# Optimization experiments

Hardware: AMD Instinct MI355X
Metric: run time of the kernel (lower is better)

## Reference

```python
import jax, jax.numpy as jnp
import numpy as np
from jax.ops import segment_sum

NUM_NODES = 100000
NUM_GRAPHS = 256


def gcn_conv(x, src, dst, W, b, num_nodes):
    """PyG GCNConv: add self-loops, symmetric deg^-1/2 normalization,
    out = scatter_add(norm * (xW)[src]) + b."""
    h = x @ W  # [N, H]
    loop = jnp.arange(num_nodes, dtype=src.dtype)
    s = jnp.concatenate([src, loop])
    d = jnp.concatenate([dst, loop])
    deg = segment_sum(jnp.ones_like(d, dtype=h.dtype), d, num_segments=num_nodes)
    dinv = jnp.where(deg > 0, jax.lax.rsqrt(deg), 0.0)
    norm = dinv[s] * dinv[d]  # [E+N]
    msg = h[s] * norm[:, None]
    return segment_sum(msg, d, num_segments=num_nodes) + b


def global_mean_pool(x, batch, num_graphs):
    summed = segment_sum(x, batch, num_segments=num_graphs)
    cnt = segment_sum(jnp.ones_like(batch, dtype=x.dtype), batch, num_segments=num_graphs)
    return summed / jnp.maximum(cnt, 1.0)[:, None]


def setup_inputs() -> dict:
    key = jax.random.key(0)
    ks = jax.random.split(key, 8)
    N, E, F_in, H = NUM_NODES, 3200000, 128, 64
    x = jax.random.normal(ks[0], (N, F_in), dtype=jnp.float32)
    edge_index = jax.random.randint(ks[1], (2, E), 0, N, dtype=jnp.int64)
    batch = jnp.sort(jax.random.randint(ks[2], (N,), 0, NUM_GRAPHS, dtype=jnp.int64))
    def glorot(k, shape):
        fan = shape[0] + shape[1]
        return jax.random.uniform(k, shape, jnp.float32, -1.0, 1.0) * np.sqrt(6.0 / fan)
    return {
        "x": x, "edge_index": edge_index, "batch": batch,
        "W1": glorot(ks[3], (F_in, H)), "b1": jnp.zeros((H,), jnp.float32),
        "W2": glorot(ks[4], (H, H)),   "b2": jnp.zeros((H,), jnp.float32),
        "W3": glorot(ks[5], (H, H)),   "b3": jnp.zeros((H,), jnp.float32),
        "Wl": glorot(ks[6], (H, 2)),   "bl": jnp.zeros((2,), jnp.float32),
    }


def reference(x, edge_index, batch, W1, b1, W2, b2, W3, b3, Wl, bl):
    src, dst = edge_index[0], edge_index[1]
    # Dropout acts as identity in eval mode; reference is deterministic.
    h = jax.nn.relu(gcn_conv(x, src, dst, W1, b1, NUM_NODES))
    h = jax.nn.relu(gcn_conv(h, src, dst, W2, b2, NUM_NODES))
    h = jax.nn.relu(gcn_conv(h, src, dst, W3, b3, NUM_NODES))
    g = global_mean_pool(h, batch, NUM_GRAPHS)  # [G, H]
    return g @ Wl + bl  # [G, 2]
```

## Files before the change

kernel.cpp:

```cpp
#include <hip/hip_runtime.h>
#include <hip/hip_bf16.h>
#include <cstdint>
#include <cstddef>

static constexpr int N_NODES = 100000;
static constexpr int N_GRAPHS = 256;
static constexpr int HF = 64;

#define SCAN_T 256
#define SCAN_E 8
#define SCAN_CHUNK (SCAN_T * SCAN_E)

#define BSHIFT 9
#define BNODES 512
#define ECHUNK 4096
#define SRCBITS 17

typedef unsigned short u16;
typedef unsigned int u32;
typedef unsigned long long u64;

__global__ void scan1_k(const int* __restrict__ in, int* __restrict__ out,
                        int* __restrict__ sums, int n) {
    __shared__ int lds[SCAN_T];
    int t = threadIdx.x;
    int base = blockIdx.x * SCAN_CHUNK + t * SCAN_E;
    int v[SCAN_E];
    int s = 0;
#pragma unroll
    for (int i = 0; i < SCAN_E; ++i) {
        int idx = base + i;
        int x = (idx < n) ? in[idx] : 0;
        v[i] = s; s += x;
    }
    lds[t] = s; __syncthreads();
    for (int off = 1; off < SCAN_T; off <<= 1) {
        int a = (t >= off) ? lds[t - off] : 0;
        __syncthreads();
        lds[t] += a;
        __syncthreads();
    }
    int excl = (t == 0) ? 0 : lds[t - 1];
    if (t == SCAN_T - 1) sums[blockIdx.x] = lds[SCAN_T - 1];
#pragma unroll
    for (int i = 0; i < SCAN_E; ++i) {
        int idx = base + i;
        if (idx < n) out[idx] = excl + v[i];
    }
}

__global__ void scan2_k(int* __restrict__ sums, int nb) {
    __shared__ int lds[SCAN_T];
    int t = threadIdx.x;
    lds[t] = (t < nb) ? sums[t] : 0;
    __syncthreads();
    for (int off = 1; off < SCAN_T; off <<= 1) {
        int a = (t >= off) ? lds[t - off] : 0;
        __syncthreads();
        lds[t] += a;
        __syncthreads();
    }
    int excl = (t == 0) ? 0 : lds[t - 1];
    if (t < nb) sums[t] = excl;
}

__global__ void scan3_k(int* __restrict__ out, const int* __restrict__ sums, int n) {
    int idx = blockIdx.x * blockDim.x + threadIdx.x;
    if (idx < n) out[idx] += sums[idx / SCAN_CHUNK];
}

__global__ void bhist_k(const int* __restrict__ dst, int* __restrict__ cnt,
                        int E, int nblk, int NB) {
    __shared__ int c[256];
    int t = threadIdx.x;
    c[t] = 0;
    __syncthreads();
    int base = blockIdx.x * ECHUNK;
    int m = min(ECHUNK, E - base);
    for (int i = t; i < m; i += 256) atomicAdd(&c[dst[base + i] >> BSHIFT], 1);
    __syncthreads();
    if (t < NB) cnt[t * nblk + blockIdx.x] = c[t];
}

__global__ void scatter_k(const int* __restrict__ src, const int* __restrict__ dst,
                          const int* __restrict__ scn, int* __restrict__ es,
                          int E, int nblk, int NB) {
    __shared__ int offs[256];
    int t = threadIdx.x;
    if (t < NB) offs[t] = scn[t * nblk + blockIdx.x];
    __syncthreads();
    int base = blockIdx.x * ECHUNK;
    int m = min(ECHUNK, E - base);
    for (int i = t; i < m; i += 256) {
        int e = base + i;
        int d = dst[e];
        int b = d >> BSHIFT;
        int p = atomicAdd(&offs[b], 1);
        es[p] = ((d & (BNODES - 1)) << SRCBITS) | src[e];
    }
}

__global__ __launch_bounds__(512) void fill2_k(const int* __restrict__ es,
                                               const int* __restrict__ scn,
                                               int* __restrict__ rowp, int* __restrict__ deg,
                                               float* __restrict__ dinv, int* __restrict__ col,
                                               int E, int nblk, int NB, int N) {
    __shared__ int ldeg[BNODES];
    __shared__ int rp[BNODES];
    __shared__ int tmp[BNODES];
    int b = blockIdx.x, t = threadIdx.x;
    int ebase = scn[b * nblk];
    int eend = (b + 1 < NB) ? scn[(b + 1) * nblk] : E;
    int d0 = b << BSHIFT;
    int nd = min(BNODES, N - d0);
    ldeg[t] = 0;
    __syncthreads();
    for (int e = ebase + t; e < eend; e += 512) atomicAdd(&ldeg[((u32)es[e]) >> SRCBITS], 1);
    __syncthreads();
    int a = ldeg[t];
    tmp[t] = a;
    __syncthreads();
    for (int off = 1; off < BNODES; off <<= 1) {
        int v = (t >= off) ? tmp[t - off] : 0;
        __syncthreads();
        tmp[t] += v;
        __syncthreads();
    }
    rp[t] = tmp[t] - a;
    __syncthreads();
    if (t < nd) {
        int d = d0 + t;
        rowp[d] = ebase + rp[t];
        deg[d] = a;
        dinv[d] = rsqrtf((float)(a + 1));
    }
    ldeg[t] = 0;
    __syncthreads();
    for (int e = ebase + t; e < eend; e += 512) {
        u32 w = (u32)es[e];
        int li = w >> SRCBITS;
        int p = atomicAdd(&ldeg[li], 1);
        col[ebase + rp[li] + p] = (int)(w & ((1u << SRCBITS) - 1));
    }
}

__global__ void wtrans_k(const float* __restrict__ W, float4* __restrict__ W4, int total) {
    int idx = blockIdx.x * blockDim.x + threadIdx.x;
    if (idx >= total) return;
    int k4 = idx >> 6, c = idx & 63;
    W4[idx] = make_float4(W[(4 * k4 + 0) * HF + c], W[(4 * k4 + 1) * HF + c],
                          W[(4 * k4 + 2) * HF + c], W[(4 * k4 + 3) * HF + c]);
}

#define DOT4(A, B, ACC) \
    ACC = fmaf((A).x, (B).x, fmaf((A).y, (B).y, fmaf((A).z, (B).z, fmaf((A).w, (B).w, (ACC)))))

template <int K>
__global__ __launch_bounds__(256, 4) void gemm6_k(const float* __restrict__ in,
                                                  const float4* __restrict__ W4,
                                                  const float* __restrict__ dinv,
                                                  __hip_bfloat16* __restrict__ u, int n) {
    __shared__ float4 Wl[16 * HF];
    __shared__ float4 Xl[64 * 17];
    int t = threadIdx.x;
    int wave = t >> 6, lane = t & 63;
    int mi = lane >> 3, ni = lane & 7;
    int qr = (wave >> 1) * 32, qc = (wave & 1) * 32;
    int rb = blockIdx.x * 64;
    float acc[4][4];
#pragma unroll
    for (int i = 0; i < 4; ++i)
#pragma unroll
        for (int j = 0; j < 4; ++j) acc[i][j] = 0.f;
    constexpr int NC = K / 64;
#pragma unroll 1
    for (int kc = 0; kc < NC; ++kc) {
        const float4* Wc = W4 + kc * 16 * HF;
#pragma unroll 1
        for (int i = t; i < 16 * HF; i += 256) Wl[i] = Wc[i];
        {
            int r = t >> 4, q = t & 15;
#pragma unroll 1
            for (int i = 0; i < 4; ++i) {
                int row = r + i * 16;
                int gr = rb + row;
                float4 v = (gr < n)
                    ? *(const float4*)(in + (size_t)gr * K + kc * 64 + q * 4)
                    : make_float4(0.f, 0.f, 0.f, 0.f);
                Xl[row * 17 + q] = v;
            }
        }
        __syncthreads();
#pragma unroll 1
        for (int k4 = 0; k4 < 16; ++k4) {
            float4 a0 = Xl[(qr + mi + 0) * 17 + k4];
            float4 a1 = Xl[(qr + mi + 8) * 17 + k4];
            float4 a2 = Xl[(qr + mi + 16) * 17 + k4];
            float4 a3 = Xl[(qr + mi + 24) * 17 + k4];
            float4 b0 = Wl[k4 * HF + qc + ni + 0];
            float4 b1 = Wl[k4 * HF + qc + ni + 8];
            float4 b2 = Wl[k4 * HF + qc + ni + 16];
            float4 b3 = Wl[k4 * HF + qc + ni + 24];
            DOT4(a0, b0, acc[0][0]); DOT4(a0, b1, acc[0][1]);
            DOT4(a0, b2, acc[0][2]); DOT4(a0, b3, acc[0][3]);
            DOT4(a1, b0, acc[1][0]); DOT4(a1, b1, acc[1][1]);
            DOT4(a1, b2, acc[1][2]); DOT4(a1, b3, acc[1][3]);
            DOT4(a2, b0, acc[2][0]); DOT4(a2, b1, acc[2][1]);
            DOT4(a2, b2, acc[2][2]); DOT4(a2, b3, acc[2][3]);
            DOT4(a3, b0, acc[3][0]); DOT4(a3, b1, acc[3][1]);
            DOT4(a3, b2, acc[3][2]); DOT4(a3, b3, acc[3][3]);
        }
        __syncthreads();
    }
#pragma unroll
    for (int i = 0; i < 4; ++i) {
        int row = rb + qr + mi + 8 * i;
        if (row < n) {
            float dv = dinv[row];
#pragma unroll
            for (int j = 0; j < 4; ++j) {
                u[(size_t)row * HF + qc + ni + 8 * j] = __float2bfloat16(acc[i][j] * dv);
            }
        }
    }
}

__global__ __launch_bounds__(256) void agg3_k(const u64* __restrict__ u,
                                              const int* __restrict__ col,
                                              const int* __restrict__ rowp,
                                              const int* __restrict__ deg,
                                              const float* __restrict__ dinv,
                                              const float* __restrict__ bias,
                                              float* __restrict__ out, int n) {
    int t = threadIdx.x;
    int ql = t & 15;
    int v = blockIdx.x * 16 + (t >> 4);
    if (v >= n) return;
    u64 q = u[(size_t)v * 16 + ql];
    u32 lo = (u32)q, hi = (u32)(q >> 32);
    float a0 = __uint_as_float(lo << 16);
    float a1 = __uint_as_float(lo & 0xffff0000u);
    float a2 = __uint_as_float(hi << 16);
    float a3 = __uint_as_float(hi & 0xffff0000u);
    int start = rowp[v];
    int nE = deg[v];
    for (int e = 0; e < nE;) {
        int m = min(16, nE - e);
        int c = (ql < m) ? col[start + e + ql] : 0;
        int i = 0;
        for (; i + 8 <= m; i += 8) {
            int s0 = __shfl(c, i, 16),     s1 = __shfl(c, i + 1, 16);
            int s2 = __shfl(c, i + 2, 16), s3 = __shfl(c, i + 3, 16);
            int s4 = __shfl(c, i + 4, 16), s5 = __shfl(c, i + 5, 16);
            int s6 = __shfl(c, i + 6, 16), s7 = __shfl(c, i + 7, 16);
            u64 q0 = u[(size_t)s0 * 16 + ql];
            u64 q1 = u[(size_t)s1 * 16 + ql];
            u64 q2 = u[(size_t)s2 * 16 + ql];
            u64 q3 = u[(size_t)s3 * 16 + ql];
            u64 q4 = u[(size_t)s4 * 16 + ql];
            u64 q5 = u[(size_t)s5 * 16 + ql];
            u64 q6 = u[(size_t)s6 * 16 + ql];
            u64 q7 = u[(size_t)s7 * 16 + ql];
            u32 l, h;
            l = (u32)q0; h = (u32)(q0 >> 32);
            a0 += __uint_as_float(l << 16); a1 += __uint_as_float(l & 0xffff0000u);
            a2 += __uint_as_float(h << 16); a3 += __uint_as_float(h & 0xffff0000u);
            l = (u32)q1; h = (u32)(q1 >> 32);
            a0 += __uint_as_float(l << 16); a1 += __uint_as_float(l & 0xffff0000u);
            a2 += __uint_as_float(h << 16); a3 += __uint_as_float(h & 0xffff0000u);
            l = (u32)q2; h = (u32)(q2 >> 32);
            a0 += __uint_as_float(l << 16); a1 += __uint_as_float(l & 0xffff0000u);
            a2 += __uint_as_float(h << 16); a3 += __uint_as_float(h & 0xffff0000u);
            l = (u32)q3; h = (u32)(q3 >> 32);
            a0 += __uint_as_float(l << 16); a1 += __uint_as_float(l & 0xffff0000u);
            a2 += __uint_as_float(h << 16); a3 += __uint_as_float(h & 0xffff0000u);
            l = (u32)q4; h = (u32)(q4 >> 32);
            a0 += __uint_as_float(l << 16); a1 += __uint_as_float(l & 0xffff0000u);
            a2 += __uint_as_float(h << 16); a3 += __uint_as_float(h & 0xffff0000u);
            l = (u32)q5; h = (u32)(q5 >> 32);
            a0 += __uint_as_float(l << 16); a1 += __uint_as_float(l & 0xffff0000u);
            a2 += __uint_as_float(h << 16); a3 += __uint_as_float(h & 0xffff0000u);
            l = (u32)q6; h = (u32)(q6 >> 32);
            a0 += __uint_as_float(l << 16); a1 += __uint_as_float(l & 0xffff0000u);
            a2 += __uint_as_float(h << 16); a3 += __uint_as_float(h & 0xffff0000u);
            l = (u32)q7; h = (u32)(q7 >> 32);
            a0 += __uint_as_float(l << 16); a1 += __uint_as_float(l & 0xffff0000u);
            a2 += __uint_as_float(h << 16); a3 += __uint_as_float(h & 0xffff0000u);
        }
        for (; i < m; ++i) {
            int s = __shfl(c, i, 16);
            u64 qq = u[(size_t)s * 16 + ql];
            u32 l = (u32)qq, h = (u32)(qq >> 32);
            a0 += __uint_as_float(l << 16);
            a1 += __uint_as_float(l & 0xffff0000u);
            a2 += __uint_as_float(h << 16);
            a3 += __uint_as_float(h & 0xffff0000u);
        }
        e += m;
    }
    float dv = dinv[v];
    float4 bb = ((const float4*)bias)[ql];
    float4 o;
    o.x = fmaxf(fmaf(a0, dv, bb.x), 0.f);
    o.y = fmaxf(fmaf(a1, dv, bb.y), 0.f);
    o.z = fmaxf(fmaf(a2, dv, bb.z), 0.f);
    o.w = fmaxf(fmaf(a3, dv, bb.w), 0.f);
    ((float4*)out)[(size_t)v * 16 + ql] = o;
}

__device__ __forceinline__ int lower_bound_i(const int* a, int n, int key) {
    int lo = 0, hi = n;
    while (lo < hi) { int mid = (lo + hi) >> 1; if (a[mid] < key) lo = mid + 1; else hi = mid; }
    return lo;
}

__global__ void pool_head_k(const float* __restrict__ h, const int* __restrict__ batch,
                            const float* __restrict__ Wl, const float* __restrict__ bl,
                            float* __restrict__ out, int n) {
    __shared__ float ssum[4][HF];
    __shared__ float smean[HF];
    int g = blockIdx.x;
    int wave = threadIdx.x >> 6, lane = threadIdx.x & 63;
    int start = lower_bound_i(batch, n, g);
    int end = lower_bound_i(batch, n, g + 1);
    float acc = 0.f;
    for (int v = start + wave; v < end; v += 4) acc += h[(size_t)v * HF + lane];
    ssum[wave][lane] = acc;
    __syncthreads();
    if (wave == 0) {
        float s = ssum[0][lane] + ssum[1][lane] + ssum[2][lane] + ssum[3][lane];
        float cnt = (float)(end - start);
        smean[lane] = s / fmaxf(cnt, 1.f);
    }
    __syncthreads();
    if (threadIdx.x < 2) {
        float o = bl[threadIdx.x];
        for (int j = 0; j < HF; ++j) o += smean[j] * Wl[j * 2 + threadIdx.x];
        out[g * 2 + threadIdx.x] = o;
    }
}

extern "C" void kernel_launch(void* const* d_in, const int* in_sizes, int n_in,
                              void* d_out, int out_size, void* d_ws, size_t ws_size,
                              hipStream_t stream) {
    const float* x     = (const float*)d_in[0];
    const int*   ei    = (const int*)d_in[1];
    const int*   batch = (const int*)d_in[2];
    const float* W1 = (const float*)d_in[3];
    const float* b1 = (const float*)d_in[4];
    const float* W2 = (const float*)d_in[5];
    const float* b2 = (const float*)d_in[6];
    const float* W3 = (const float*)d_in[7];
    const float* b3 = (const float*)d_in[8];
    const float* Wl = (const float*)d_in[9];
    const float* bl = (const float*)d_in[10];
    float* outp = (float*)d_out;

    const int N = N_NODES;
    const int E = in_sizes[1] / 2;
    const int NB = (N + BNODES - 1) >> BSHIFT;
    const int NBLK = (E + ECHUNK - 1) / ECHUNK;
    const int M = NB * NBLK;

    char* ws = (char*)d_ws;
    size_t off = 0;
    auto alloc = [&](size_t bytes) {
        void* p = ws + off;
        off = (off + bytes + 255) & ~size_t(255);
        return p;
    };
    size_t ubytes = (size_t)N * HF * 2;
    if ((size_t)E * 4 > ubytes) ubytes = (size_t)E * 4;
    float*  P    = (float*)alloc((size_t)N * HF * 4);
    void*   Uv   = alloc(ubytes);
    int*    colA = (int*)alloc((size_t)E * 4);
    int*    deg  = (int*)alloc((size_t)N * 4);
    float*  dinv = (float*)alloc((size_t)N * 4);
    int*    rowp = (int*)alloc((size_t)N * 4);
    int*    cnt  = (int*)alloc((size_t)M * 4);
    int*    scn  = (int*)alloc((size_t)M * 4);
    int*    sums = (int*)alloc(4096);
    float4* W4_1 = (float4*)alloc((size_t)(128 / 4) * HF * 16);
    float4* W4_2 = (float4*)alloc((size_t)(64 / 4) * HF * 16);
    float4* W4_3 = (float4*)alloc((size_t)(64 / 4) * HF * 16);
    __hip_bfloat16* U = (__hip_bfloat16*)Uv;
    u64* U64 = (u64*)Uv;
    int* es  = (int*)Uv;
    (void)ws_size; (void)n_in; (void)out_size;

    const int* src = ei;
    const int* dst = ei + E;

    bhist_k<<<NBLK, 256, 0, stream>>>(dst, cnt, E, NBLK, NB);
    int nb = (M + SCAN_CHUNK - 1) / SCAN_CHUNK;
    scan1_k<<<nb, SCAN_T, 0, stream>>>(cnt, scn, sums, M);
    scan2_k<<<1, SCAN_T, 0, stream>>>(sums, nb);
    scan3_k<<<(M + 255) / 256, 256, 0, stream>>>(scn, sums, M);
    scatter_k<<<NBLK, 256, 0, stream>>>(src, dst, scn, es, E, NBLK, NB);
    fill2_k<<<NB, 512, 0, stream>>>(es, scn, rowp, deg, dinv, colA, E, NBLK, NB, N);

    wtrans_k<<<(32 * HF + 255) / 256, 256, 0, stream>>>(W1, W4_1, 32 * HF);
    wtrans_k<<<(16 * HF + 255) / 256, 256, 0, stream>>>(W2, W4_2, 16 * HF);
    wtrans_k<<<(16 * HF + 255) / 256, 256, 0, stream>>>(W3, W4_3, 16 * HF);

    int gRow16 = (N + 15) / 16;
    int gRow64 = (N + 63) / 64;
    gemm6_k<128><<<gRow64, 256, 0, stream>>>(x, W4_1, dinv, U, N);
    agg3_k<<<gRow16, 256, 0, stream>>>(U64, colA, rowp, deg, dinv, b1, P, N);
    gemm6_k<64><<<gRow64, 256, 0, stream>>>(P, W4_2, dinv, U, N);
    agg3_k<<<gRow16, 256, 0, stream>>>(U64, colA, rowp, deg, dinv, b2, P, N);
    gemm6_k<64><<<gRow64, 256, 0, stream>>>(P, W4_3, dinv, U, N);
    agg3_k<<<gRow16, 256, 0, stream>>>(U64, colA, rowp, deg, dinv, b3, P, N);

    pool_head_k<<<N_GRAPHS, 256, 0, stream>>>(P, batch, Wl, bl, outp, N);
}
```

Measured before the change: 350.8 us.

## Use 16-byte gathers in aggregation, fold scan fixup and merge weight transposes

The aggregation kernel now assigns 8 lanes per node, each loading a 16-byte uint4 of bf16 features and accumulating 8 channels. Previously 16 lanes each loaded 8 bytes. The change is meant to halve gather instruction count and pack more nodes per wave. The separate scan fixup kernel is removed by adding block sums at the consumer reads in scatter and fill. The three weight-transpose launches are merged into one. Registers per thread rise with eight accumulators, and edge batching is now 8 per iteration.

```diff
diff --git a/kernel.cpp b/kernel.cpp
--- a/kernel.cpp
+++ b/kernel.cpp
@@ -10,6 +10,7 @@
 #define SCAN_T 256
 #define SCAN_E 8
 #define SCAN_CHUNK (SCAN_T * SCAN_E)
+#define SCAN_SHIFT 11
 
 #define BSHIFT 9
 #define BNODES 512
@@ -64,11 +65,6 @@
     if (t < nb) sums[t] = excl;
 }
 
-__global__ void scan3_k(int* __restrict__ out, const int* __restrict__ sums, int n) {
-    int idx = blockIdx.x * blockDim.x + threadIdx.x;
-    if (idx < n) out[idx] += sums[idx / SCAN_CHUNK];
-}
-
 __global__ void bhist_k(const int* __restrict__ dst, int* __restrict__ cnt,
                         int E, int nblk, int NB) {
     __shared__ int c[256];
@@ -83,11 +79,14 @@
 }
 
 __global__ void scatter_k(const int* __restrict__ src, const int* __restrict__ dst,
-                          const int* __restrict__ scn, int* __restrict__ es,
-                          int E, int nblk, int NB) {
+                          const int* __restrict__ scn, const int* __restrict__ sums,
+                          int* __restrict__ es, int E, int nblk, int NB) {
     __shared__ int offs[256];
     int t = threadIdx.x;
-    if (t < NB) offs[t] = scn[t * nblk + blockIdx.x];
+    if (t < NB) {
+        int i = t * nblk + blockIdx.x;
+        offs[t] = scn[i] + sums[i >> SCAN_SHIFT];
+    }
     __syncthreads();
     int base = blockIdx.x * ECHUNK;
     int m = min(ECHUNK, E - base);
@@ -102,6 +101,7 @@
 
 __global__ __launch_bounds__(512) void fill2_k(const int* __restrict__ es,
                                                const int* __restrict__ scn,
+                                               const int* __restrict__ sums,
                                                int* __restrict__ rowp, int* __restrict__ deg,
                                                float* __restrict__ dinv, int* __restrict__ col,
                                                int E, int nblk, int NB, int N) {
@@ -109,8 +109,15 @@
     __shared__ int rp[BNODES];
     __shared__ int tmp[BNODES];
     int b = blockIdx.x, t = threadIdx.x;
-    int ebase = scn[b * nblk];
-    int eend = (b + 1 < NB) ? scn[(b + 1) * nblk] : E;
+    int i0 = b * nblk;
+    int ebase = scn[i0] + sums[i0 >> SCAN_SHIFT];
+    int eend;
+    if (b + 1 < NB) {
+        int i1 = (b + 1) * nblk;
+        eend = scn[i1] + sums[i1 >> SCAN_SHIFT];
+    } else {
+        eend = E;
+    }
     int d0 = b << BSHIFT;
     int nd = min(BNODES, N - d0);
     ldeg[t] = 0;
@@ -144,12 +151,19 @@
     }
 }
 
-__global__ void wtrans_k(const float* __restrict__ W, float4* __restrict__ W4, int total) {
+__global__ void wtrans3_k(const float* __restrict__ W1, float4* __restrict__ W4_1,
+                          const float* __restrict__ W2, float4* __restrict__ W4_2,
+                          const float* __restrict__ W3, float4* __restrict__ W4_3) {
     int idx = blockIdx.x * blockDim.x + threadIdx.x;
-    if (idx >= total) return;
-    int k4 = idx >> 6, c = idx & 63;
-    W4[idx] = make_float4(W[(4 * k4 + 0) * HF + c], W[(4 * k4 + 1) * HF + c],
-                          W[(4 * k4 + 2) * HF + c], W[(4 * k4 + 3) * HF + c]);
+    const float* W;
+    float4* W4;
+    int li;
+    if (idx < 2048)      { W = W1; W4 = W4_1; li = idx; }
+    else if (idx < 3072) { W = W2; W4 = W4_2; li = idx - 2048; }
+    else                 { W = W3; W4 = W4_3; li = idx - 3072; }
+    int k4 = li >> 6, c = li & 63;
+    W4[li] = make_float4(W[(4 * k4 + 0) * HF + c], W[(4 * k4 + 1) * HF + c],
+                         W[(4 * k4 + 2) * HF + c], W[(4 * k4 + 3) * HF + c]);
 }
 
 #define DOT4(A, B, ACC) \
@@ -225,7 +239,15 @@
     }
 }
 
-__global__ __launch_bounds__(256) void agg3_k(const u64* __restrict__ u,
+#define UNPACK_ADD(Q)                                                       \
+    do {                                                                    \
+        a0 += __uint_as_float((Q).x << 16); a1 += __uint_as_float((Q).x & 0xffff0000u); \
+        a2 += __uint_as_float((Q).y << 16); a3 += __uint_as_float((Q).y & 0xffff0000u); \
+        a4 += __uint_as_float((Q).z << 16); a5 += __uint_as_float((Q).z & 0xffff0000u); \
+        a6 += __uint_as_float((Q).w << 16); a7 += __uint_as_float((Q).w & 0xffff0000u); \
+    } while (0)
+
+__global__ __launch_bounds__(256) void agg4_k(const uint4* __restrict__ u,
                                               const int* __restrict__ col,
                                               const int* __restrict__ rowp,
                                               const int* __restrict__ deg,
@@ -233,79 +255,57 @@
                                               const float* __restrict__ bias,
                                               float* __restrict__ out, int n) {
     int t = threadIdx.x;
-    int ql = t & 15;
-    int v = blockIdx.x * 16 + (t >> 4);
+    int el = t & 7;
+    int v = blockIdx.x * 32 + (t >> 3);
     if (v >= n) return;
-    u64 q = u[(size_t)v * 16 + ql];
-    u32 lo = (u32)q, hi = (u32)(q >> 32);
-    float a0 = __uint_as_float(lo << 16);
-    float a1 = __uint_as_float(lo & 0xffff0000u);
-    float a2 = __uint_as_float(hi << 16);
-    float a3 = __uint_as_float(hi & 0xffff0000u);
+    uint4 q = u[(size_t)v * 8 + el];
+    float a0 = __uint_as_float(q.x << 16), a1 = __uint_as_float(q.x & 0xffff0000u);
+    float a2 = __uint_as_float(q.y << 16), a3 = __uint_as_float(q.y & 0xffff0000u);
+    float a4 = __uint_as_float(q.z << 16), a5 = __uint_as_float(q.z & 0xffff0000u);
+    float a6 = __uint_as_float(q.w << 16), a7 = __uint_as_float(q.w & 0xffff0000u);
     int start = rowp[v];
     int nE = deg[v];
     for (int e = 0; e < nE;) {
-        int m = min(16, nE - e);
-        int c = (ql < m) ? col[start + e + ql] : 0;
-        int i = 0;
-        for (; i + 8 <= m; i += 8) {
-            int s0 = __shfl(c, i, 16),     s1 = __shfl(c, i + 1, 16);
-            int s2 = __shfl(c, i + 2, 16), s3 = __shfl(c, i + 3, 16);
-            int s4 = __shfl(c, i + 4, 16), s5 = __shfl(c, i + 5, 16);
-            int s6 = __shfl(c, i + 6, 16), s7 = __shfl(c, i + 7, 16);
-            u64 q0 = u[(size_t)s0 * 16 + ql];
-            u64 q1 = u[(size_t)s1 * 16 + ql];
-            u64 q2 = u[(size_t)s2 * 16 + ql];
-            u64 q3 = u[(size_t)s3 * 16 + ql];
-            u64 q4 = u[(size_t)s4 * 16 + ql];
-            u64 q5 = u[(size_t)s5 * 16 + ql];
-            u64 q6 = u[(size_t)s6 * 16 + ql];
-            u64 q7 = u[(size_t)s7 * 16 + ql];
-            u32 l, h;
-            l = (u32)q0; h = (u32)(q0 >> 32);
-            a0 += __uint_as_float(l << 16); a1 += __uint_as_float(l & 0xffff0000u);
-            a2 += __uint_as_float(h << 16); a3 += __uint_as_float(h & 0xffff0000u);
-            l = (u32)q1; h = (u32)(q1 >> 32);
-            a0 += __uint_as_float(l << 16); a1 += __uint_as_float(l & 0xffff0000u);
-            a2 += __uint_as_float(h << 16); a3 += __uint_as_float(h & 0xffff0000u);
-            l = (u32)q2; h = (u32)(q2 >> 32);
-            a0 += __uint_as_float(l << 16); a1 += __uint_as_float(l & 0xffff0000u);
-            a2 += __uint_as_float(h << 16); a3 += __uint_as_float(h & 0xffff0000u);
-            l = (u32)q3; h = (u32)(q3 >> 32);
-            a0 += __uint_as_float(l << 16); a1 += __uint_as_float(l & 0xffff0000u);
-            a2 += __uint_as_float(h << 16); a3 += __uint_as_float(h & 0xffff0000u);
-            l = (u32)q4; h = (u32)(q4 >> 32);
-            a0 += __uint_as_float(l << 16); a1 += __uint_as_float(l & 0xffff0000u);
-            a2 += __uint_as_float(h << 16); a3 += __uint_as_float(h & 0xffff0000u);
-            l = (u32)q5; h = (u32)(q5 >> 32);
-            a0 += __uint_as_float(l << 16); a1 += __uint_as_float(l & 0xffff0000u);
-            a2 += __uint_as_float(h << 16); a3 += __uint_as_float(h & 0xffff0000u);
-            l = (u32)q6; h = (u32)(q6 >> 32);
-            a0 += __uint_as_float(l << 16); a1 += __uint_as_float(l & 0xffff0000u);
-            a2 += __uint_as_float(h << 16); a3 += __uint_as_float(h & 0xffff0000u);
-            l = (u32)q7; h = (u32)(q7 >> 32);
-            a0 += __uint_as_float(l << 16); a1 += __uint_as_float(l & 0xffff0000u);
-            a2 += __uint_as_float(h << 16); a3 += __uint_as_float(h & 0xffff0000u);
-        }
-        for (; i < m; ++i) {
-            int s = __shfl(c, i, 16);
-            u64 qq = u[(size_t)s * 16 + ql];
-            u32 l = (u32)qq, h = (u32)(qq >> 32);
-            a0 += __uint_as_float(l << 16);
-            a1 += __uint_as_float(l & 0xffff0000u);
-            a2 += __uint_as_float(h << 16);
-            a3 += __uint_as_float(h & 0xffff0000u);
+        int m = min(8, nE - e);
+        int c = (el < m) ? col[start + e + el] : 0;
+        if (m == 8) {
+            int s0 = __shfl(c, 0, 8), s1 = __shfl(c, 1, 8);
+            int s2 = __shfl(c, 2, 8), s3 = __shfl(c, 3, 8);
+            int s4 = __shfl(c, 4, 8), s5 = __shfl(c, 5, 8);
+            int s6 = __shfl(c, 6, 8), s7 = __shfl(c, 7, 8);
+            uint4 q0 = u[(size_t)s0 * 8 + el];
+            uint4 q1 = u[(size_t)s1 * 8 + el];
+            uint4 q2 = u[(size_t)s2 * 8 + el];
+            uint4 q3 = u[(size_t)s3 * 8 + el];
+            uint4 q4 = u[(size_t)s4 * 8 + el];
+            uint4 q5 = u[(size_t)s5 * 8 + el];
+            uint4 q6 = u[(size_t)s6 * 8 + el];
+            uint4 q7 = u[(size_t)s7 * 8 + el];
+            UNPACK_ADD(q0); UNPACK_ADD(q1); UNPACK_ADD(q2); UNPACK_ADD(q3);
+            UNPACK_ADD(q4); UNPACK_ADD(q5); UNPACK_ADD(q6); UNPACK_ADD(q7);
+        } else {
+            for (int i = 0; i < m; ++i) {
+                int s = __shfl(c, i, 8);
+                uint4 qq = u[(size_t)s * 8 + el];
+                UNPACK_ADD(qq);
+            }
         }
         e += m;
     }
     float dv = dinv[v];
-    float4 bb = ((const float4*)bias)[ql];
-    float4 o;
-    o.x = fmaxf(fmaf(a0, dv, bb.x), 0.f);
-    o.y = fmaxf(fmaf(a1, dv, bb.y), 0.f);
-    o.z = fmaxf(fmaf(a2, dv, bb.z), 0.f);
-    o.w = fmaxf(fmaf(a3, dv, bb.w), 0.f);
-    ((float4*)out)[(size_t)v * 16 + ql] = o;
+    float4 b0 = ((const float4*)bias)[2 * el];
+    float4 b1 = ((const float4*)bias)[2 * el + 1];
+    float4 o0, o1;
+    o0.x = fmaxf(fmaf(a0, dv, b0.x), 0.f);
+    o0.y = fmaxf(fmaf(a1, dv, b0.y), 0.f);
+    o0.z = fmaxf(fmaf(a2, dv, b0.z), 0.f);
+    o0.w = fmaxf(fmaf(a3, dv, b0.w), 0.f);
+    o1.x = fmaxf(fmaf(a4, dv, b1.x), 0.f);
+    o1.y = fmaxf(fmaf(a5, dv, b1.y), 0.f);
+    o1.z = fmaxf(fmaf(a6, dv, b1.z), 0.f);
+    o1.w = fmaxf(fmaf(a7, dv, b1.w), 0.f);
+    ((float4*)out)[(size_t)v * 16 + 2 * el] = o0;
+    ((float4*)out)[(size_t)v * 16 + 2 * el + 1] = o1;
 }
 
 __device__ __forceinline__ int lower_bound_i(const int* a, int n, int key) {
@@ -384,7 +384,7 @@
     float4* W4_2 = (float4*)alloc((size_t)(64 / 4) * HF * 16);
     float4* W4_3 = (float4*)alloc((size_t)(64 / 4) * HF * 16);
     __hip_bfloat16* U = (__hip_bfloat16*)Uv;
-    u64* U64 = (u64*)Uv;
+    uint4* U4 = (uint4*)Uv;
     int* es  = (int*)Uv;
     (void)ws_size; (void)n_in; (void)out_size;
 
@@ -395,22 +395,19 @@
     int nb = (M + SCAN_CHUNK - 1) / SCAN_CHUNK;
     scan1_k<<<nb, SCAN_T, 0, stream>>>(cnt, scn, sums, M);
     scan2_k<<<1, SCAN_T, 0, stream>>>(sums, nb);
-    scan3_k<<<(M + 255) / 256, 256, 0, stream>>>(scn, sums, M);
-    scatter_k<<<NBLK, 256, 0, stream>>>(src, dst, scn, es, E, NBLK, NB);
-    fill2_k<<<NB, 512, 0, stream>>>(es, scn, rowp, deg, dinv, colA, E, NBLK, NB, N);
-
-    wtrans_k<<<(32 * HF + 255) / 256, 256, 0, stream>>>(W1, W4_1, 32 * HF);
-    wtrans_k<<<(16 * HF + 255) / 256, 256, 0, stream>>>(W2, W4_2, 16 * HF);
-    wtrans_k<<<(16 * HF + 255) / 256, 256, 0, stream>>>(W3, W4_3, 16 * HF);
-
-    int gRow16 = (N + 15) / 16;
+    scatter_k<<<NBLK, 256, 0, stream>>>(src, dst, scn, sums, es, E, NBLK, NB);
+    fill2_k<<<NB, 512, 0, stream>>>(es, scn, sums, rowp, deg, dinv, colA, E, NBLK, NB, N);
+
+    wtrans3_k<<<16, 256, 0, stream>>>(W1, W4_1, W2, W4_2, W3, W4_3);
+
+    int gRow32 = (N + 31) / 32;
     int gRow64 = (N + 63) / 64;
     gemm6_k<128><<<gRow64, 256, 0, stream>>>(x, W4_1, dinv, U, N);
-    agg3_k<<<gRow16, 256, 0, stream>>>(U64, colA, rowp, deg, dinv, b1, P, N);
+    agg4_k<<<gRow32, 256, 0, stream>>>(U4, colA, rowp, deg, dinv, b1, P, N);
     gemm6_k<64><<<gRow64, 256, 0, stream>>>(P, W4_2, dinv, U, N);
-    agg3_k<<<gRow16, 256, 0, stream>>>(U64, colA, rowp, deg, dinv, b2, P, N);
+    agg4_k<<<gRow32, 256, 0, stream>>>(U4, colA, rowp, deg, dinv, b2, P, N);
     gemm6_k<64><<<gRow64, 256, 0, stream>>>(P, W4_3, dinv, U, N);
-    agg3_k<<<gRow16, 256, 0, stream>>>(U64, colA, rowp, deg, dinv, b3, P, N);
+    agg4_k<<<gRow32, 256, 0, stream>>>(U4, colA, rowp, deg, dinv, b3, P, N);
 
     pool_head_k<<<N_GRAPHS, 256, 0, stream>>>(P, batch, Wl, bl, outp, N);
 }
```

Result: slower. 379.0 us (+8.0%).
